# Performance work log

Hardware: AMD Instinct MI355X
Metric: run time of the kernel (lower is better)

Reference implementation:

```python
import jax, jax.numpy as jnp
import numpy as np

N, K, D = 200000, 512, 128
N_ITER = 3
BETA = 1e-3
EPS = 1e-10


def setup_inputs() -> dict:
    key = jax.random.key(0)
    k1, k2 = jax.random.split(key)
    x = jax.random.normal(k1, (N, D), dtype=jnp.float32)
    centers = 0.1 * jax.random.normal(k2, (K, D), dtype=jnp.float32)  # torch 'random' init: 0.1*randn([K, D])
    return {"x": x, "centers": centers}


def reference(x, centers):
    # Iterative soft k-means (SOPL). dist[n,k] = ||x_n - c_k||^2, computed as
    x_sq = jnp.sum(x * x, axis=-1, keepdims=True)  # [N, 1]
    for _ in range(N_ITER):
        c_sq = jnp.sum(centers * centers, axis=-1)  # [K]
        dist = x_sq - 2.0 * (x @ centers.T) + c_sq  # [N, K]
        w = jax.nn.softmax(-dist / BETA, axis=-1)   # soft assignments, [N, K]
        num = w.T @ x                                # [K, D] weighted sum
        den = jnp.sum(w, axis=0)[:, None] + EPS      # [K, 1] soft counts
        centers = num / den
    return centers
```

## Files before the change

### kernel.cpp

```cpp
#include <hip/hip_runtime.h>

#define N_PTS 200000
#define KC    512
#define DIM   128
#define NITER 3
#define EPS   1e-10
#define BETA  1e-3
#define PWIN  0.35f
#define ACUT  -32.0
#define LCAND 16
#define NSUB  8
#define SUBCAP 512
#define CSTRIDE 16

typedef __attribute__((ext_vector_type(8)))  short short8;
typedef __attribute__((ext_vector_type(16))) float f32x16;

__device__ inline unsigned short f2bf(float f) {
    unsigned u = __float_as_uint(f);
    unsigned r = u + 0x7FFFu + ((u >> 16) & 1u);
    return (unsigned short)(r >> 16);
}


__global__ void k_packx(const float* __restrict__ x, short8* __restrict__ Xf) {
    int pt = blockIdx.x;
    int tid = threadIdx.x;
    int lane = tid & 63, g = tid >> 6;
    int row = pt * 32 + (lane & 31);
    int koff = (lane >> 5) * 8;
    #pragma unroll
    for (int kk = 0; kk < 2; ++kk) {
        int kb = g * 2 + kk;
        short8 v;
        #pragma unroll
        for (int i = 0; i < 8; ++i)
            ((unsigned short*)&v)[i] = f2bf(x[(size_t)row * DIM + kb * 16 + koff + i]);
        Xf[((size_t)pt * 8 + kb) * 64 + lane] = v;
    }
}

__global__ void k_init(const float* __restrict__ cin, double* __restrict__ Cf64,
                       unsigned short* __restrict__ Cfrag, double* __restrict__ csqd,
                       float* __restrict__ csqf, double* __restrict__ num,
                       double* __restrict__ den, unsigned* __restrict__ cursor) {
    int k = blockIdx.x, d = threadIdx.x;
    float v = cin[k * DIM + d];
    double c = (double)v;
    Cf64[(size_t)k * DIM + d] = c;
    num[(size_t)k * DIM + d] = 0.0;
    if (d < NSUB) cursor[((size_t)k * NSUB + d) * CSTRIDE] = 0u;
    int ct = k >> 5, kb = d >> 4, j = d & 15;
    int lane = (k & 31) + 32 * (j >> 3);
    Cfrag[(((size_t)ct * 8 + kb) * 64 + lane) * 8 + (j & 7)] = f2bf(v);
    double p = c * c;
    #pragma unroll
    for (int m = 1; m < 64; m <<= 1) p += __shfl_xor(p, m);
    __shared__ double ps[2];
    if ((d & 63) == 0) ps[d >> 6] = p;
    __syncthreads();
    if (d == 0) {
        double s = ps[0] + ps[1];
        csqd[k] = s; csqf[k] = (float)s;
        den[k] = 0.0;
    }
}

__launch_bounds__(256)
__global__ void k_dense(const float* __restrict__ x, const short8* __restrict__ Xf,
                        const short8* __restrict__ Cfrag, const float* __restrict__ csqf,
                        const double* __restrict__ Cf64, const double* __restrict__ csqd,
                        unsigned* __restrict__ cursor,
                        unsigned* __restrict__ entries_n, double* __restrict__ entries_w) {
    __shared__ float rowmin_w[4][32];
    __shared__ float rowmin_s[32];
    __shared__ int   ccnt[32];
    __shared__ unsigned short clist[32][LCAND];
    __shared__ int   wl[32];
    __shared__ int   wlcnt;

    const int tid = threadIdx.x;
    const int wv = tid >> 6, lane = tid & 63;
    const int blk = blockIdx.x;
    const int sub = blk & (NSUB - 1);

    short8 a[8];
    #pragma unroll
    for (int kb = 0; kb < 8; ++kb)
        a[kb] = Xf[((size_t)blk * 8 + kb) * 64 + lane];

    float dd[4][16];
    #pragma unroll
    for (int t = 0; t < 4; ++t) {
        int ct = wv * 4 + t;
        f32x16 acc;
        #pragma unroll
        for (int r = 0; r < 16; ++r) acc[r] = 0.0f;
        #pragma unroll
        for (int kb = 0; kb < 8; ++kb) {
            short8 b = Cfrag[((size_t)ct * 8 + kb) * 64 + lane];
            acc = __builtin_amdgcn_mfma_f32_32x32x16_bf16(a[kb], b, acc, 0, 0, 0);
        }
        float cq = csqf[ct * 32 + (lane & 31)];
        #pragma unroll
        for (int r = 0; r < 16; ++r) dd[t][r] = cq - 2.0f * acc[r];
    }

    float mt[16];
    #pragma unroll
    for (int r = 0; r < 16; ++r) {
        float m = fminf(fminf(dd[0][r], dd[1][r]), fminf(dd[2][r], dd[3][r]));
        #pragma unroll
        for (int s = 16; s >= 1; s >>= 1) m = fminf(m, __shfl_xor(m, s));
        mt[r] = m;
    }
    if ((lane & 31) == 0) {
        int h = lane >> 5;
        #pragma unroll
        for (int r = 0; r < 16; ++r)
            rowmin_w[wv][(r & 3) + 8 * (r >> 2) + 4 * h] = mt[r];
    }
    __syncthreads();
    if (tid < 32) {
        rowmin_s[tid] = fminf(fminf(rowmin_w[0][tid], rowmin_w[1][tid]),
                              fminf(rowmin_w[2][tid], rowmin_w[3][tid]));
        ccnt[tid] = 0;
    }
    if (tid == 0) wlcnt = 0;
    __syncthreads();

    {
        const int h = lane >> 5;
        #pragma unroll
        for (int t = 0; t < 4; ++t) {
            int ct = wv * 4 + t;
            #pragma unroll
            for (int r = 0; r < 16; ++r) {
                int row = (r & 3) + 8 * (r >> 2) + 4 * h;
                if (dd[t][r] - rowmin_s[row] < PWIN) {
                    int idx = atomicAdd(&ccnt[row], 1);
                    if (idx < LCAND)
                        clist[row][idx] = (unsigned short)(ct * 32 + (lane & 31));
                }
            }
        }
    }
    __syncthreads();

    {
        int p = wv * 8 + (lane & 7);
        if (lane < 8 && ccnt[p] == 1) {
            int k = clist[p][0];
            size_t base = (size_t)k * NSUB + sub;
            unsigned pos = atomicAdd(&cursor[base * CSTRIDE], 1u);
            if (pos < SUBCAP) {
                entries_n[base * SUBCAP + pos] = (unsigned)(blk * 32 + p);
                entries_w[base * SUBCAP + pos] = 1.0;
            }
        }
    }
    if (tid < 32 && ccnt[tid] > 1) {
        int i = atomicAdd(&wlcnt, 1);
        wl[i] = tid;
    }
    __syncthreads();

    int nwl = wlcnt;
    for (int i = wv; i < nwl; i += 4) {
        int p = wl[i];
        int n = blk * 32 + p;
        int cnt = ccnt[p]; if (cnt > LCAND) cnt = LCAND;

        double xa = (double)x[(size_t)n * DIM + lane];
        double xb = (double)x[(size_t)n * DIM + 64 + lane];

        double myd = 1e300; int myk = -1;
        for (int c = 0; c < cnt; ++c) {
            int k = clist[p][c];
            double pr = xa * Cf64[(size_t)k * DIM + lane] + xb * Cf64[(size_t)k * DIM + 64 + lane];
            #pragma unroll
            for (int m = 1; m < 64; m <<= 1) pr += __shfl_xor(pr, m);
            double dist = csqd[k] - 2.0 * pr;
            if (lane == c) { myd = dist; myk = k; }
        }
        double md = myd;
        #pragma unroll
        for (int m = 1; m < 64; m <<= 1) md = fmin(md, __shfl_xor(md, m));
        double zm = -md / BETA;
        double arg = (myk >= 0) ? (-myd / BETA - zm) : -1e300;
        double e = (myk >= 0) ? exp(arg) : 0.0;
        double esum = e;
        #pragma unroll
        for (int m = 1; m < 64; m <<= 1) esum += __shfl_xor(esum, m);

        if (myk >= 0 && arg >= ACUT) {
            double wgt = e / esum;
            size_t base = (size_t)myk * NSUB + sub;
            unsigned pos = atomicAdd(&cursor[base * CSTRIDE], 1u);
            if (pos < SUBCAP) {
                entries_n[base * SUBCAP + pos] = (unsigned)n;
                entries_w[base * SUBCAP + pos] = wgt;
            }
        }
    }
}

__global__ void k_reduce(const float* __restrict__ x, const unsigned* __restrict__ cursor,
                         const unsigned* __restrict__ entries_n,
                         const double* __restrict__ entries_w,
                         double* __restrict__ num, double* __restrict__ den) {
    int b = blockIdx.x;
    int k = b >> 2, part = b & 3;
    int d = threadIdx.x;

    double a0 = 0.0, a1 = 0.0, a2 = 0.0, a3 = 0.0, ws = 0.0;
    #pragma unroll
    for (int s = 0; s < 2; ++s) {
        int sub = part * 2 + s;
        size_t base = (size_t)k * NSUB + sub;
        unsigned len = cursor[base * CSTRIDE]; if (len > SUBCAP) len = SUBCAP;
        const unsigned* en = entries_n + base * SUBCAP;
        const double*   ew = entries_w + base * SUBCAP;
        unsigned e = 0;
        for (; e + 4 <= len; e += 4) {
            unsigned n0 = en[e], n1 = en[e + 1], n2 = en[e + 2], n3 = en[e + 3];
            double w0 = ew[e], w1 = ew[e + 1], w2 = ew[e + 2], w3 = ew[e + 3];
            float f0 = x[(size_t)n0 * DIM + d];
            float f1 = x[(size_t)n1 * DIM + d];
            float f2 = x[(size_t)n2 * DIM + d];
            float f3 = x[(size_t)n3 * DIM + d];
            a0 += w0 * (double)f0; a1 += w1 * (double)f1;
            a2 += w2 * (double)f2; a3 += w3 * (double)f3;
            ws += ((w0 + w1) + (w2 + w3));
        }
        for (; e < len; ++e) {
            unsigned n0 = en[e]; double w0 = ew[e];
            a0 += w0 * (double)x[(size_t)n0 * DIM + d];
            ws += w0;
        }
    }
    double acc = (a0 + a1) + (a2 + a3);
    atomicAdd(&num[(size_t)k * DIM + d], acc);
    if (d == 0) atomicAdd(&den[k], ws);
}

__global__ void k_update(double* __restrict__ num, double* __restrict__ den,
                         double* __restrict__ Cf64, unsigned short* __restrict__ Cfrag,
                         double* __restrict__ csqd, float* __restrict__ csqf,
                         unsigned* __restrict__ cursor, float* __restrict__ out, int last) {
    int k = blockIdx.x, d = threadIdx.x;
    double nv = num[(size_t)k * DIM + d];
    double dv = den[k] + EPS;
    double c = nv / dv;
    Cf64[(size_t)k * DIM + d] = c;
    num[(size_t)k * DIM + d] = 0.0;
    if (d < NSUB) cursor[((size_t)k * NSUB + d) * CSTRIDE] = 0u;
    if (last) out[k * DIM + d] = (float)c;
    int ct = k >> 5, kb = d >> 4, j = d & 15;
    int lane = (k & 31) + 32 * (j >> 3);
    Cfrag[(((size_t)ct * 8 + kb) * 64 + lane) * 8 + (j & 7)] = f2bf((float)c);
    double p = c * c;
    #pragma unroll
    for (int m = 1; m < 64; m <<= 1) p += __shfl_xor(p, m);
    __shared__ double ps[2];
    if ((d & 63) == 0) ps[d >> 6] = p;
    __syncthreads();
    if (d == 0) {
        double s = ps[0] + ps[1];
        csqd[k] = s; csqf[k] = (float)s;
        den[k] = 0.0;
    }
}

extern "C" void kernel_launch(void* const* d_in, const int* in_sizes, int n_in,
                              void* d_out, int out_size, void* d_ws, size_t ws_size,
                              hipStream_t stream) {
    const float* x   = (const float*)d_in[0];
    const float* cin = (const float*)d_in[1];
    float* out = (float*)d_out;

    char* w = (char*)d_ws;
    size_t off = 0;
    auto alloc = [&](size_t bytes) -> void* {
        void* p = w + off;
        off = (off + bytes + 255) & ~(size_t)255;
        return p;
    };
    double*         Cf64   = (double*)alloc((size_t)KC * DIM * 8);
    unsigned short* Cfrag  = (unsigned short*)alloc((size_t)KC * DIM * 2);
    double*         csqd   = (double*)alloc((size_t)KC * 8);
    float*          csqf   = (float*)alloc((size_t)KC * 4);
    double*         num    = (double*)alloc((size_t)KC * DIM * 8);
    double*         den    = (double*)alloc((size_t)KC * 8);
    unsigned*       cursor = (unsigned*)alloc((size_t)KC * NSUB * CSTRIDE * 4);
    unsigned*       entries_n = (unsigned*)alloc((size_t)KC * NSUB * SUBCAP * 4);
    double*         entries_w = (double*)alloc((size_t)KC * NSUB * SUBCAP * 8);
    short8*         Xf     = (short8*)alloc((size_t)N_PTS * DIM * 2);
    (void)ws_size; (void)in_sizes; (void)n_in; (void)out_size;

    hipLaunchKernelGGL(k_init, dim3(KC), dim3(DIM), 0, stream,
                       cin, Cf64, Cfrag, csqd, csqf, num, den, cursor);
    hipLaunchKernelGGL(k_packx, dim3(N_PTS / 32), dim3(256), 0, stream, x, Xf);

    for (int it = 0; it < NITER; ++it) {
        hipLaunchKernelGGL(k_dense, dim3(N_PTS / 32), dim3(256), 0, stream,
                           x, Xf, (const short8*)Cfrag, csqf, Cf64, csqd,
                           cursor, entries_n, entries_w);
        hipLaunchKernelGGL(k_reduce, dim3(KC * 4), dim3(DIM), 0, stream,
                           x, cursor, entries_n, entries_w, num, den);
        hipLaunchKernelGGL(k_update, dim3(KC), dim3(DIM), 0, stream,
                           num, den, Cf64, Cfrag, csqd, csqf, cursor, out,
                           (it == NITER - 1) ? 1 : 0);
    }
}
```

Before: 500.4 us.

## Give each wavefront its own 32-point tile in dense distance pass

Restructures k_dense so that each of the four wavefronts in a block owns an independent 32-point tile and loops over all 16 center tiles, instead of the four waves splitting the centers of one shared tile. The row minimum is tracked as a running min, and the bf16 MFMA GEMM is then recomputed in a second pass to select candidates, so the 64-float dd array no longer has to stay live in registers. This also removes the block-wide __syncthreads and replaces the shared worklist with a per-wave ballot loop. The cost is twice the MFMA work and the Cfrag loads, in exchange for lower register pressure, higher occupancy (launch bounds of 4) and no cross-wave synchronisation.

Result: slower. 525.1 us (+4.9%).

```diff
diff --git a/kernel.cpp b/kernel.cpp
--- a/kernel.cpp
+++ b/kernel.cpp
@@ -12,6 +12,7 @@
 #define NSUB  8
 #define SUBCAP 512
 #define CSTRIDE 16
+#define NTILE (N_PTS / 32)
 
 typedef __attribute__((ext_vector_type(8)))  short short8;
 typedef __attribute__((ext_vector_type(16))) float f32x16;
@@ -66,33 +67,32 @@
     }
 }
 
-__launch_bounds__(256)
+__launch_bounds__(256, 4)
 __global__ void k_dense(const float* __restrict__ x, const short8* __restrict__ Xf,
                         const short8* __restrict__ Cfrag, const float* __restrict__ csqf,
                         const double* __restrict__ Cf64, const double* __restrict__ csqd,
                         unsigned* __restrict__ cursor,
                         unsigned* __restrict__ entries_n, double* __restrict__ entries_w) {
-    __shared__ float rowmin_w[4][32];
-    __shared__ float rowmin_s[32];
-    __shared__ int   ccnt[32];
-    __shared__ unsigned short clist[32][LCAND];
-    __shared__ int   wl[32];
-    __shared__ int   wlcnt;
+    __shared__ float          rowmin_s[4][32];
+    __shared__ int            ccnt[4][32];
+    __shared__ unsigned short clist[4][32][LCAND];
 
     const int tid = threadIdx.x;
     const int wv = tid >> 6, lane = tid & 63;
-    const int blk = blockIdx.x;
-    const int sub = blk & (NSUB - 1);
+    const int tile = blockIdx.x * 4 + wv;
+    if (tile >= NTILE) return;
+    const int sub = tile & (NSUB - 1);
+    const int h = lane >> 5;
 
     short8 a[8];
     #pragma unroll
     for (int kb = 0; kb < 8; ++kb)
-        a[kb] = Xf[((size_t)blk * 8 + kb) * 64 + lane];
-
-    float dd[4][16];
-    #pragma unroll
-    for (int t = 0; t < 4; ++t) {
-        int ct = wv * 4 + t;
+        a[kb] = Xf[((size_t)tile * 8 + kb) * 64 + lane];
+
+    float runmin[16];
+    #pragma unroll
+    for (int r = 0; r < 16; ++r) runmin[r] = 1e30f;
+    for (int ct = 0; ct < 16; ++ct) {
         f32x16 acc;
         #pragma unroll
         for (int r = 0; r < 16; ++r) acc[r] = 0.0f;
@@ -103,80 +103,67 @@
         }
         float cq = csqf[ct * 32 + (lane & 31)];
         #pragma unroll
-        for (int r = 0; r < 16; ++r) dd[t][r] = cq - 2.0f * acc[r];
-    }
-
-    float mt[16];
+        for (int r = 0; r < 16; ++r) runmin[r] = fminf(runmin[r], cq - 2.0f * acc[r]);
+    }
     #pragma unroll
     for (int r = 0; r < 16; ++r) {
-        float m = fminf(fminf(dd[0][r], dd[1][r]), fminf(dd[2][r], dd[3][r]));
+        float m = runmin[r];
         #pragma unroll
         for (int s = 16; s >= 1; s >>= 1) m = fminf(m, __shfl_xor(m, s));
-        mt[r] = m;
+        runmin[r] = m;
     }
     if ((lane & 31) == 0) {
-        int h = lane >> 5;
         #pragma unroll
         for (int r = 0; r < 16; ++r)
-            rowmin_w[wv][(r & 3) + 8 * (r >> 2) + 4 * h] = mt[r];
-    }
-    __syncthreads();
-    if (tid < 32) {
-        rowmin_s[tid] = fminf(fminf(rowmin_w[0][tid], rowmin_w[1][tid]),
-                              fminf(rowmin_w[2][tid], rowmin_w[3][tid]));
-        ccnt[tid] = 0;
-    }
-    if (tid == 0) wlcnt = 0;
-    __syncthreads();
-
-    {
-        const int h = lane >> 5;
-        #pragma unroll
-        for (int t = 0; t < 4; ++t) {
-            int ct = wv * 4 + t;
-            #pragma unroll
-            for (int r = 0; r < 16; ++r) {
-                int row = (r & 3) + 8 * (r >> 2) + 4 * h;
-                if (dd[t][r] - rowmin_s[row] < PWIN) {
-                    int idx = atomicAdd(&ccnt[row], 1);
-                    if (idx < LCAND)
-                        clist[row][idx] = (unsigned short)(ct * 32 + (lane & 31));
-                }
+            rowmin_s[wv][(r & 3) + 8 * (r >> 2) + 4 * h] = runmin[r];
+    }
+    if (lane < 32) ccnt[wv][lane] = 0;
+
+    for (int ct = 0; ct < 16; ++ct) {
+        f32x16 acc;
+        #pragma unroll
+        for (int r = 0; r < 16; ++r) acc[r] = 0.0f;
+        #pragma unroll
+        for (int kb = 0; kb < 8; ++kb) {
+            short8 b = Cfrag[((size_t)ct * 8 + kb) * 64 + lane];
+            acc = __builtin_amdgcn_mfma_f32_32x32x16_bf16(a[kb], b, acc, 0, 0, 0);
+        }
+        float cq = csqf[ct * 32 + (lane & 31)];
+        #pragma unroll
+        for (int r = 0; r < 16; ++r) {
+            float ddv = cq - 2.0f * acc[r];
+            int row = (r & 3) + 8 * (r >> 2) + 4 * h;
+            if (ddv - rowmin_s[wv][row] < PWIN) {
+                int idx = atomicAdd(&ccnt[wv][row], 1);
+                if (idx < LCAND)
+                    clist[wv][row][idx] = (unsigned short)(ct * 32 + (lane & 31));
             }
         }
     }
-    __syncthreads();
-
-    {
-        int p = wv * 8 + (lane & 7);
-        if (lane < 8 && ccnt[p] == 1) {
-            int k = clist[p][0];
-            size_t base = (size_t)k * NSUB + sub;
-            unsigned pos = atomicAdd(&cursor[base * CSTRIDE], 1u);
-            if (pos < SUBCAP) {
-                entries_n[base * SUBCAP + pos] = (unsigned)(blk * 32 + p);
-                entries_w[base * SUBCAP + pos] = 1.0;
-            }
-        }
-    }
-    if (tid < 32 && ccnt[tid] > 1) {
-        int i = atomicAdd(&wlcnt, 1);
-        wl[i] = tid;
-    }
-    __syncthreads();
-
-    int nwl = wlcnt;
-    for (int i = wv; i < nwl; i += 4) {
-        int p = wl[i];
-        int n = blk * 32 + p;
-        int cnt = ccnt[p]; if (cnt > LCAND) cnt = LCAND;
+
+    if (lane < 32 && ccnt[wv][lane] == 1) {
+        int k = clist[wv][lane][0];
+        size_t base = (size_t)k * NSUB + sub;
+        unsigned pos = atomicAdd(&cursor[base * CSTRIDE], 1u);
+        if (pos < SUBCAP) {
+            entries_n[base * SUBCAP + pos] = (unsigned)(tile * 32 + lane);
+            entries_w[base * SUBCAP + pos] = 1.0;
+        }
+    }
+
+    unsigned long long rmask = __ballot(lane < 32 && ccnt[wv][lane] > 1);
+    while (rmask) {
+        int p = __ffsll(rmask) - 1;
+        rmask &= rmask - 1;
+        int n = tile * 32 + p;
+        int cnt = ccnt[wv][p]; if (cnt > LCAND) cnt = LCAND;
 
         double xa = (double)x[(size_t)n * DIM + lane];
         double xb = (double)x[(size_t)n * DIM + 64 + lane];
 
         double myd = 1e300; int myk = -1;
         for (int c = 0; c < cnt; ++c) {
-            int k = clist[p][c];
+            int k = clist[wv][p][c];
             double pr = xa * Cf64[(size_t)k * DIM + lane] + xb * Cf64[(size_t)k * DIM + 64 + lane];
             #pragma unroll
             for (int m = 1; m < 64; m <<= 1) pr += __shfl_xor(pr, m);
@@ -300,10 +287,10 @@
 
     hipLaunchKernelGGL(k_init, dim3(KC), dim3(DIM), 0, stream,
                        cin, Cf64, Cfrag, csqd, csqf, num, den, cursor);
-    hipLaunchKernelGGL(k_packx, dim3(N_PTS / 32), dim3(256), 0, stream, x, Xf);
+    hipLaunchKernelGGL(k_packx, dim3(NTILE), dim3(256), 0, stream, x, Xf);
 
     for (int it = 0; it < NITER; ++it) {
-        hipLaunchKernelGGL(k_dense, dim3(N_PTS / 32), dim3(256), 0, stream,
+        hipLaunchKernelGGL(k_dense, dim3((NTILE + 3) / 4), dim3(256), 0, stream,
                            x, Xf, (const short8*)Cfrag, csqf, Cf64, csqd,
                            cursor, entries_n, entries_w);
         hipLaunchKernelGGL(k_reduce, dim3(KC * 4), dim3(DIM), 0, stream,
```
